# Kernel optimization log

Measured on AMD Instinct MI355X. Metric: run time of the kernel, lower is better.

## Reference

```python
import jax, jax.numpy as jnp
import numpy as np

B, S, D = 2, 2048, 2048
NQ, NKV = 16, 4
HD = D // NQ           # 128
GROUP = NQ // NKV      # 4


def setup_inputs() -> dict:
    key = jax.random.key(0)
    k_x, k_q, k_k, k_v, k_o = jax.random.split(key, 5)
    scale = 0.02
    return {
        "x": jax.random.normal(k_x, (B, S, D), dtype=jnp.float32),
        # torch nn.Linear weights have shape (out_features, in_features)
        "Wq": jax.random.normal(k_q, (D, D), dtype=jnp.float32) * scale,
        "Wk": jax.random.normal(k_k, (NKV * HD, D), dtype=jnp.float32) * scale,
        "Wv": jax.random.normal(k_v, (NKV * HD, D), dtype=jnp.float32) * scale,
        "Wo": jax.random.normal(k_o, (D, D), dtype=jnp.float32) * scale,
    }


def reference(x, Wq, Wk, Wv, Wo):
    b, s, _ = x.shape
    # projections (Linear: x @ W.T), then split heads -> (b, h, s, hd)
    Q = (x @ Wq.T).reshape(b, s, NQ, HD).transpose(0, 2, 1, 3)
    K = (x @ Wk.T).reshape(b, s, NKV, HD).transpose(0, 2, 1, 3)
    V = (x @ Wv.T).reshape(b, s, NKV, HD).transpose(0, 2, 1, 3)
    # GQA: broadcast each KV head across its query-head group (repeat_interleave on head dim)
    K = jnp.repeat(K, GROUP, axis=1)  # (b, NQ, s, hd)
    V = jnp.repeat(V, GROUP, axis=1)
    scores = jnp.einsum("bhqd,bhkd->bhqk", Q, K) / jnp.sqrt(jnp.float32(HD))
    causal = jnp.triu(jnp.ones((s, s), dtype=bool), k=1)  # True above diagonal -> masked
    scores = jnp.where(causal, -jnp.inf, scores)
    weights = jax.nn.softmax(scores, axis=-1)  # dropout p=0.0 -> identity
    ctx = jnp.einsum("bhqk,bhkd->bhqd", weights, V)
    ctx = ctx.transpose(0, 2, 1, 3).reshape(b, s, D)
    return ctx @ Wo.T
```

## Files before the change

kernel.cpp:

```cpp
#include <hip/hip_runtime.h>
#include <stdint.h>

#define S_LEN 2048
#define DMODEL 2048
#define NQH 16
#define NKVH 4
#define HDK 128

typedef __bf16 bf16x8 __attribute__((ext_vector_type(8)));
typedef float f32x4 __attribute__((ext_vector_type(4)));
typedef float f32x16 __attribute__((ext_vector_type(16)));

__device__ __forceinline__ void async16(const void* g, void* l) {
  __builtin_amdgcn_global_load_lds((const __attribute__((address_space(1))) void*)g,
                                   (__attribute__((address_space(3))) void*)l,
                                   16, 0, 0);
}

__device__ __forceinline__ f32x4 mfma16(bf16x8 a, bf16x8 b, f32x4 c) {
  return __builtin_amdgcn_mfma_f32_16x16x32_bf16(a, b, c, 0, 0, 0);
}
__device__ __forceinline__ f32x16 mfma32(bf16x8 a, bf16x8 b, f32x16 c) {
  return __builtin_amdgcn_mfma_f32_32x32x16_bf16(a, b, c, 0, 0, 0);
}
__device__ __forceinline__ uint32_t pkbf16(float lo, float hi) {
  uint32_t r;
  asm("v_cvt_pk_bf16_f32 %0, %1, %2" : "=v"(r) : "v"(lo), "v"(hi));
  return r;
}

__global__ __launch_bounds__(256) void cvt_all(
    const float* __restrict__ i0, const float* __restrict__ i1,
    const float* __restrict__ i2, const float* __restrict__ i3,
    const float* __restrict__ i4, __bf16* __restrict__ o0,
    __bf16* __restrict__ o1, __bf16* __restrict__ o2, __bf16* __restrict__ o3,
    __bf16* __restrict__ o4) {
  int v = blockIdx.x * 256 + threadIdx.x;
  const float* in;
  __bf16* out;
  int base;
  if (v < 1048576)      { in = i0; out = o0; base = 0; }
  else if (v < 1572864) { in = i1; out = o1; base = 1048576; }
  else if (v < 1703936) { in = i2; out = o2; base = 1572864; }
  else if (v < 1835008) { in = i3; out = o3; base = 1703936; }
  else                  { in = i4; out = o4; base = 1835008; }
  int i = (v - base) * 8;
  const float4* p = (const float4*)(in + i);
  float4 a = p[0], b = p[1];
  bf16x8 o;
  o[0] = (__bf16)a.x; o[1] = (__bf16)a.y; o[2] = (__bf16)a.z; o[3] = (__bf16)a.w;
  o[4] = (__bf16)b.x; o[5] = (__bf16)b.y; o[6] = (__bf16)b.z; o[7] = (__bf16)b.w;
  *(bf16x8*)(out + i) = o;
}

template <bool F32OUT, bool VSEG2>
__global__ __launch_bounds__(256) void gemm_bt(const __bf16* __restrict__ A,
                                               const __bf16* __restrict__ B0,
                                               const __bf16* __restrict__ B1,
                                               const __bf16* __restrict__ B2,
                                               void* __restrict__ C0,
                                               void* __restrict__ C1,
                                               void* __restrict__ C2,
                                               int Ntot, int Ns1, int Ns2, int K) {
  int nbn = Ntot >> 7;
  int nwg = gridDim.x;
  int bid = blockIdx.x;
  int bx = (bid & 7) * (nwg >> 3) + (bid >> 3);
  int m0 = (bx / nbn) << 7;
  int n0g = (bx % nbn) << 7;
  const __bf16* B;
  void* C;
  int n0, Nc;
  bool seg2 = false;
  if (n0g < Ns1)      { B = B0; C = C0; n0 = n0g;       Nc = Ns1; }
  else if (n0g < Ns2) { B = B1; C = C1; n0 = n0g - Ns1; Nc = Ns2 - Ns1; }
  else                { B = B2; C = C2; n0 = n0g - Ns2; Nc = Ntot - Ns2; seg2 = true; }

  __shared__ __align__(16) uint8_t As[16384];
  __shared__ __align__(16) uint8_t Bs[16384];

  int t = threadIdx.x, lane = t & 63, w = t >> 6;
  int wr = w >> 1, wc = w & 1;
  f32x4 acc[4][4] = {};

  for (int k0 = 0; k0 < K; k0 += 64) {
#pragma unroll
    for (int i = 0; i < 4; ++i) {
      int c = (i << 8) + t;
      int row = c >> 3;
      int colb = ((c & 7) << 4) ^ ((row & 7) << 4);
      async16((const uint8_t*)(A + (size_t)(m0 + row) * K + k0) + colb, As + c * 16);
      async16((const uint8_t*)(B + (size_t)(n0 + row) * K + k0) + colb, Bs + c * 16);
    }
    __syncthreads();
#pragma unroll
    for (int ks = 0; ks < 2; ++ks) {
      bf16x8 af[4], bfr[4];
#pragma unroll
      for (int m = 0; m < 4; ++m) {
        int row = wr * 64 + m * 16 + (lane & 15);
        int colb = ((ks << 6) + ((lane >> 4) << 4)) ^ ((row & 7) << 4);
        af[m] = *(const bf16x8*)(As + row * 128 + colb);
      }
#pragma unroll
      for (int n = 0; n < 4; ++n) {
        int row = wc * 64 + n * 16 + (lane & 15);
        int colb = ((ks << 6) + ((lane >> 4) << 4)) ^ ((row & 7) << 4);
        bfr[n] = *(const bf16x8*)(Bs + row * 128 + colb);
      }
      __builtin_amdgcn_s_setprio(1);
#pragma unroll
      for (int m = 0; m < 4; ++m)
#pragma unroll
        for (int n = 0; n < 4; ++n)
          acc[m][n] = mfma16(af[m], bfr[n], acc[m][n]);
      __builtin_amdgcn_s_setprio(0);
    }
    __syncthreads();
  }
#pragma unroll
  for (int m = 0; m < 4; ++m)
#pragma unroll
    for (int n = 0; n < 4; ++n)
#pragma unroll
      for (int j = 0; j < 4; ++j) {
        int mg = m0 + wr * 64 + m * 16 + ((lane >> 4) << 2) + j;
        int ng = n0 + wc * 64 + n * 16 + (lane & 15);
        float v = acc[m][n][j];
        if (VSEG2 && seg2) {
          int bb = mg >> 11, s = mg & 2047;
          size_t vidx = ((size_t)((bb << 2) + (ng >> 7)) * 32 + (s >> 6)) * 8192 +
                        (size_t)((s >> 2) & 15) * 512 + (size_t)(ng & 127) * 4 +
                        (s & 3);
          ((__bf16*)C)[vidx] = (__bf16)v;
        } else if (F32OUT) {
          ((float*)C)[(size_t)mg * Nc + ng] = v;
        } else {
          ((__bf16*)C)[(size_t)mg * Nc + ng] = (__bf16)v;
        }
      }
}

__global__ __launch_bounds__(256, 2) void attn(const __bf16* __restrict__ Q,
                                               const __bf16* __restrict__ Kx,
                                               const __bf16* __restrict__ Vt,
                                               __bf16* __restrict__ Ctx) {
  int bid0 = blockIdx.x;
  int bid = ((bid0 & 7) << 6) | (bid0 >> 3);
  int qt = 15 - (bid & 15);
  int h = (bid >> 4) & 15;
  int b = bid >> 8;
  int kvh = h >> 2;
  int q0 = qt << 7;
  int t = threadIdx.x, lane = t & 63, w = t >> 6;
  int qr = lane & 31;
  int hi = lane >> 5;
  int qwb = q0 + (w << 5);

  __shared__ __align__(16) uint8_t Ks[2][16384];
  __shared__ __align__(16) uint8_t Vs[2][16384];

  const __bf16* kbase = Kx + (size_t)b * S_LEN * 512 + kvh * HDK;
  const __bf16* vbase = Vt + (size_t)(b * NKVH + kvh) * 32 * 8192;

  auto stage = [&](int kt, int bufi) {
#pragma unroll
    for (int i = 0; i < 4; ++i) {
      int c = (i << 8) + t;
      int krow = c >> 4;
      int kcolb = ((c & 15) << 4) ^ ((krow & 7) << 4);
      async16((const uint8_t*)(kbase + (size_t)((kt << 6) + krow) * 512) + kcolb,
              Ks[bufi] + c * 16);
      async16((const uint8_t*)(vbase + (size_t)kt * 8192) + c * 16,
              Vs[bufi] + c * 16);
    }
  };

  int NT = (qt << 1) + 2;
  stage(0, 0);

  bf16x8 qf[8];
  {
    const __bf16* qrow = Q + (size_t)(b * S_LEN + qwb + qr) * DMODEL + h * HDK + hi * 8;
#pragma unroll
    for (int dk = 0; dk < 8; ++dk) qf[dk] = *(const bf16x8*)(qrow + dk * 16);
  }
  __syncthreads();

  const float NEG = -3.0e38f;
  const float SC = 0.08838834764831845f;
  float m_run = NEG, l_run = 0.f;
  f32x16 acc[4] = {};

  for (int kt = 0; kt < NT; ++kt) {
    int cur = kt & 1;
    if (kt + 1 < NT) stage(kt + 1, cur ^ 1);
    int k0 = kt << 6;
    if (k0 <= qwb + 31) {
      const uint8_t* ks = Ks[cur];
      const uint8_t* vs = Vs[cur];

      f32x16 st0 = {}, st1 = {};
      __builtin_amdgcn_s_setprio(1);
#pragma unroll
      for (int dk = 0; dk < 8; ++dk) {
        int cb = (dk << 5) + (hi << 4);
        int swz = (qr & 7) << 4;
        bf16x8 kf0 = *(const bf16x8*)(ks + qr * 256 + (cb ^ swz));
        st0 = mfma32(kf0, qf[dk], st0);
        bf16x8 kf1 = *(const bf16x8*)(ks + (32 + qr) * 256 + (cb ^ swz));
        st1 = mfma32(kf1, qf[dk], st1);
      }
      __builtin_amdgcn_s_setprio(0);

      if (k0 + 63 > qwb) {
#pragma unroll
        for (int r = 0; r < 16; ++r) {
          int kl = (r & 3) + ((r >> 2) << 3) + (hi << 2);
          st0[r] = (k0 + kl > qwb + qr) ? NEG : st0[r];
          st1[r] = (k0 + 32 + kl > qwb + qr) ? NEG : st1[r];
        }
      }

      float tm[16];
#pragma unroll
      for (int r = 0; r < 16; ++r) tm[r] = fmaxf(st0[r], st1[r]);
#pragma unroll
      for (int s = 8; s > 0; s >>= 1)
#pragma unroll
        for (int r = 0; r < s; ++r) tm[r] = fmaxf(tm[r], tm[r + s]);
      float mx = fmaxf(tm[0], __shfl_xor(tm[0], 32, 64));

      if (__any(mx > m_run + 90.52f)) {
        float mn = fmaxf(m_run, mx);
        float al = __expf((m_run - mn) * SC);
        l_run *= al;
        m_run = mn;
#pragma unroll
        for (int i = 0; i < 16; ++i) {
          float alr = __shfl(al, (i & 3) + ((i >> 2) << 3) + (hi << 2), 64);
          acc[0][i] *= alr; acc[1][i] *= alr; acc[2][i] *= alr; acc[3][i] *= alr;
        }
      }

      float mSC = m_run * SC;
      float p0[16], p1[16];
#pragma unroll
      for (int r = 0; r < 16; ++r) p0[r] = __expf(fmaf(st0[r], SC, -mSC));
#pragma unroll
      for (int r = 0; r < 16; ++r) p1[r] = __expf(fmaf(st1[r], SC, -mSC));
      float ts[16];
#pragma unroll
      for (int r = 0; r < 16; ++r) ts[r] = p0[r] + p1[r];
#pragma unroll
      for (int s = 8; s > 0; s >>= 1)
#pragma unroll
        for (int r = 0; r < s; ++r) ts[r] += ts[r + s];
      l_run += ts[0];

      bf16x8 pa[4];
      {
        union { bf16x8 v; uint32_t u[4]; } t0, t1, t2, t3;
#pragma unroll
        for (int i = 0; i < 4; ++i) {
          t0.u[i] = pkbf16(p0[2 * i], p0[2 * i + 1]);
          t1.u[i] = pkbf16(p0[8 + 2 * i], p0[9 + 2 * i]);
          t2.u[i] = pkbf16(p1[2 * i], p1[2 * i + 1]);
          t3.u[i] = pkbf16(p1[8 + 2 * i], p1[9 + 2 * i]);
        }
        pa[0] = t0.v; pa[1] = t1.v; pa[2] = t2.v; pa[3] = t3.v;
      }

      __builtin_amdgcn_s_setprio(1);
#pragma unroll
      for (int dt = 0; dt < 4; ++dt) {
        int row = (dt << 5) + qr;
#pragma unroll
        for (int kc = 0; kc < 4; ++kc) {
          int g0 = (kc << 2) + hi;
          union { bf16x8 v; uint64_t q[2]; } vfu;
          vfu.q[0] = *(const uint64_t*)(vs + (g0 << 10) + (row << 3));
          vfu.q[1] = *(const uint64_t*)(vs + ((g0 + 2) << 10) + (row << 3));
          acc[dt] = mfma32(pa[kc], vfu.v, acc[dt]);
        }
      }
      __builtin_amdgcn_s_setprio(0);
    }
    __syncthreads();
  }

  l_run += __shfl_xor(l_run, 32, 64);
#pragma unroll
  for (int i = 0; i < 16; ++i) {
    int rm = (i & 3) + ((i >> 2) << 3) + (hi << 2);
    float lr = __shfl(l_run, rm, 64);
    float inv = 1.0f / lr;
    size_t rowoff = (size_t)(b * S_LEN + qwb + rm) * DMODEL + h * HDK + qr;
#pragma unroll
    for (int dt = 0; dt < 4; ++dt)
      Ctx[rowoff + (dt << 5)] = (__bf16)(acc[dt][i] * inv);
  }
}

extern "C" void kernel_launch(void* const* d_in, const int* in_sizes, int n_in,
                              void* d_out, int out_size, void* d_ws, size_t ws_size,
                              hipStream_t stream) {
  const float* x  = (const float*)d_in[0];
  const float* Wq = (const float*)d_in[1];
  const float* Wk = (const float*)d_in[2];
  const float* Wv = (const float*)d_in[3];
  const float* Wo = (const float*)d_in[4];
  float* out = (float*)d_out;

  const size_t MB = 1024 * 1024;
  uint8_t* ws = (uint8_t*)d_ws;
  __bf16* xb  = (__bf16*)(ws + 0 * MB);
  __bf16* Wqb = (__bf16*)(ws + 16 * MB);
  __bf16* Wkb = (__bf16*)(ws + 24 * MB);
  __bf16* Wvb = (__bf16*)(ws + 26 * MB);
  __bf16* Wob = (__bf16*)(ws + 28 * MB);
  __bf16* Qb  = (__bf16*)(ws + 36 * MB);
  __bf16* Kb  = (__bf16*)(ws + 52 * MB);
  __bf16* Vtb = (__bf16*)(ws + 60 * MB);
  __bf16* Ctx = (__bf16*)(ws + 64 * MB);

  cvt_all<<<9216, 256, 0, stream>>>(x, Wq, Wk, Wv, Wo, xb, Wqb, Wkb, Wvb, Wob);

  gemm_bt<false, true><<<(4096 / 128) * (3072 / 128), 256, 0, stream>>>(
      xb, Wqb, Wkb, Wvb, (void*)Qb, (void*)Kb, (void*)Vtb, 3072, 2048, 2560, 2048);

  attn<<<512, 256, 0, stream>>>(Qb, Kb, Vtb, Ctx);

  gemm_bt<true, false><<<(4096 / 128) * (2048 / 128), 256, 0, stream>>>(
      Ctx, Wob, Wob, Wob, (void*)out, (void*)out, (void*)out, 2048, 2048, 2048, 2048);
}
```

Measured before the change: 191.7 us.

## Software-pipeline QK of next tile with softmax and PV of current tile

Restructures the causal attention loop so that the QK^T MFMAs for tile kt+1 are issued alongside the softmax and PV work for tile kt. To support this, K and V staging are split: K is prefetched two tiles ahead and V one tile ahead. The loop is unrolled by two so the score register sets alternate. The aim is to hide exp/reduction latency behind matrix-core work, at the cost of two extra 16-float accumulator sets per lane, which raises register pressure and may lower occupancy.

```diff
diff --git a/kernel.cpp b/kernel.cpp
--- a/kernel.cpp
+++ b/kernel.cpp
@@ -163,21 +163,29 @@
   const __bf16* kbase = Kx + (size_t)b * S_LEN * 512 + kvh * HDK;
   const __bf16* vbase = Vt + (size_t)(b * NKVH + kvh) * 32 * 8192;
 
-  auto stage = [&](int kt, int bufi) {
+  auto stageK = [&](int kt, int slot) {
 #pragma unroll
     for (int i = 0; i < 4; ++i) {
       int c = (i << 8) + t;
       int krow = c >> 4;
       int kcolb = ((c & 15) << 4) ^ ((krow & 7) << 4);
       async16((const uint8_t*)(kbase + (size_t)((kt << 6) + krow) * 512) + kcolb,
-              Ks[bufi] + c * 16);
+              Ks[slot] + c * 16);
+    }
+  };
+  auto stageV = [&](int kt, int slot) {
+#pragma unroll
+    for (int i = 0; i < 4; ++i) {
+      int c = (i << 8) + t;
       async16((const uint8_t*)(vbase + (size_t)kt * 8192) + c * 16,
-              Vs[bufi] + c * 16);
+              Vs[slot] + c * 16);
     }
   };
 
   int NT = (qt << 1) + 2;
-  stage(0, 0);
+  stageK(0, 0);
+  stageV(0, 0);
+  stageK(1, 1);
 
   bf16x8 qf[8];
   {
@@ -189,104 +197,117 @@
 
   const float NEG = -3.0e38f;
   const float SC = 0.08838834764831845f;
+  const f32x16 vzero = {};
   float m_run = NEG, l_run = 0.f;
   f32x16 acc[4] = {};
 
-  for (int kt = 0; kt < NT; ++kt) {
-    int cur = kt & 1;
-    if (kt + 1 < NT) stage(kt + 1, cur ^ 1);
+  auto qk = [&](int kt, f32x16& n0, f32x16& n1) {
+    const uint8_t* ks = Ks[kt & 1];
+    n0 = vzero; n1 = vzero;
+    int swz = (qr & 7) << 4;
+    __builtin_amdgcn_s_setprio(1);
+#pragma unroll
+    for (int dk = 0; dk < 8; ++dk) {
+      int cb = (dk << 5) + (hi << 4);
+      bf16x8 kf0 = *(const bf16x8*)(ks + qr * 256 + (cb ^ swz));
+      n0 = mfma32(kf0, qf[dk], n0);
+      bf16x8 kf1 = *(const bf16x8*)(ks + (32 + qr) * 256 + (cb ^ swz));
+      n1 = mfma32(kf1, qf[dk], n1);
+    }
+    __builtin_amdgcn_s_setprio(0);
     int k0 = kt << 6;
-    if (k0 <= qwb + 31) {
-      const uint8_t* ks = Ks[cur];
-      const uint8_t* vs = Vs[cur];
-
-      f32x16 st0 = {}, st1 = {};
-      __builtin_amdgcn_s_setprio(1);
-#pragma unroll
-      for (int dk = 0; dk < 8; ++dk) {
-        int cb = (dk << 5) + (hi << 4);
-        int swz = (qr & 7) << 4;
-        bf16x8 kf0 = *(const bf16x8*)(ks + qr * 256 + (cb ^ swz));
-        st0 = mfma32(kf0, qf[dk], st0);
-        bf16x8 kf1 = *(const bf16x8*)(ks + (32 + qr) * 256 + (cb ^ swz));
-        st1 = mfma32(kf1, qf[dk], st1);
-      }
-      __builtin_amdgcn_s_setprio(0);
-
-      if (k0 + 63 > qwb) {
-#pragma unroll
-        for (int r = 0; r < 16; ++r) {
-          int kl = (r & 3) + ((r >> 2) << 3) + (hi << 2);
-          st0[r] = (k0 + kl > qwb + qr) ? NEG : st0[r];
-          st1[r] = (k0 + 32 + kl > qwb + qr) ? NEG : st1[r];
-        }
-      }
-
-      float tm[16];
-#pragma unroll
-      for (int r = 0; r < 16; ++r) tm[r] = fmaxf(st0[r], st1[r]);
-#pragma unroll
-      for (int s = 8; s > 0; s >>= 1)
-#pragma unroll
-        for (int r = 0; r < s; ++r) tm[r] = fmaxf(tm[r], tm[r + s]);
-      float mx = fmaxf(tm[0], __shfl_xor(tm[0], 32, 64));
-
-      if (__any(mx > m_run + 90.52f)) {
-        float mn = fmaxf(m_run, mx);
-        float al = __expf((m_run - mn) * SC);
-        l_run *= al;
-        m_run = mn;
-#pragma unroll
-        for (int i = 0; i < 16; ++i) {
-          float alr = __shfl(al, (i & 3) + ((i >> 2) << 3) + (hi << 2), 64);
-          acc[0][i] *= alr; acc[1][i] *= alr; acc[2][i] *= alr; acc[3][i] *= alr;
-        }
-      }
-
-      float mSC = m_run * SC;
-      float p0[16], p1[16];
-#pragma unroll
-      for (int r = 0; r < 16; ++r) p0[r] = __expf(fmaf(st0[r], SC, -mSC));
-#pragma unroll
-      for (int r = 0; r < 16; ++r) p1[r] = __expf(fmaf(st1[r], SC, -mSC));
-      float ts[16];
-#pragma unroll
-      for (int r = 0; r < 16; ++r) ts[r] = p0[r] + p1[r];
-#pragma unroll
-      for (int s = 8; s > 0; s >>= 1)
-#pragma unroll
-        for (int r = 0; r < s; ++r) ts[r] += ts[r + s];
-      l_run += ts[0];
-
-      bf16x8 pa[4];
-      {
-        union { bf16x8 v; uint32_t u[4]; } t0, t1, t2, t3;
-#pragma unroll
-        for (int i = 0; i < 4; ++i) {
-          t0.u[i] = pkbf16(p0[2 * i], p0[2 * i + 1]);
-          t1.u[i] = pkbf16(p0[8 + 2 * i], p0[9 + 2 * i]);
-          t2.u[i] = pkbf16(p1[2 * i], p1[2 * i + 1]);
-          t3.u[i] = pkbf16(p1[8 + 2 * i], p1[9 + 2 * i]);
-        }
-        pa[0] = t0.v; pa[1] = t1.v; pa[2] = t2.v; pa[3] = t3.v;
-      }
-
-      __builtin_amdgcn_s_setprio(1);
-#pragma unroll
-      for (int dt = 0; dt < 4; ++dt) {
-        int row = (dt << 5) + qr;
-#pragma unroll
-        for (int kc = 0; kc < 4; ++kc) {
-          int g0 = (kc << 2) + hi;
-          union { bf16x8 v; uint64_t q[2]; } vfu;
-          vfu.q[0] = *(const uint64_t*)(vs + (g0 << 10) + (row << 3));
-          vfu.q[1] = *(const uint64_t*)(vs + ((g0 + 2) << 10) + (row << 3));
-          acc[dt] = mfma32(pa[kc], vfu.v, acc[dt]);
-        }
-      }
-      __builtin_amdgcn_s_setprio(0);
-    }
+    if (k0 + 63 > qwb) {
+#pragma unroll
+      for (int r = 0; r < 16; ++r) {
+        int kl = (r & 3) + ((r >> 2) << 3) + (hi << 2);
+        n0[r] = (k0 + kl > qwb + qr) ? NEG : n0[r];
+        n1[r] = (k0 + 32 + kl > qwb + qr) ? NEG : n1[r];
+      }
+    }
+  };
+
+  auto smpv = [&](int kt, f32x16& c0, f32x16& c1) {
+    float tm[16];
+#pragma unroll
+    for (int r = 0; r < 16; ++r) tm[r] = fmaxf(c0[r], c1[r]);
+#pragma unroll
+    for (int s = 8; s > 0; s >>= 1)
+#pragma unroll
+      for (int r = 0; r < s; ++r) tm[r] = fmaxf(tm[r], tm[r + s]);
+    float mx = fmaxf(tm[0], __shfl_xor(tm[0], 32, 64));
+
+    if (__any(mx > m_run + 90.52f)) {
+      float mn = fmaxf(m_run, mx);
+      float al = __expf((m_run - mn) * SC);
+      l_run *= al;
+      m_run = mn;
+#pragma unroll
+      for (int i = 0; i < 16; ++i) {
+        float alr = __shfl(al, (i & 3) + ((i >> 2) << 3) + (hi << 2), 64);
+        acc[0][i] *= alr; acc[1][i] *= alr; acc[2][i] *= alr; acc[3][i] *= alr;
+      }
+    }
+
+    float mSC = m_run * SC;
+    float p0[16], p1[16];
+#pragma unroll
+    for (int r = 0; r < 16; ++r) p0[r] = __expf(fmaf(c0[r], SC, -mSC));
+#pragma unroll
+    for (int r = 0; r < 16; ++r) p1[r] = __expf(fmaf(c1[r], SC, -mSC));
+    float ts[16];
+#pragma unroll
+    for (int r = 0; r < 16; ++r) ts[r] = p0[r] + p1[r];
+#pragma unroll
+    for (int s = 8; s > 0; s >>= 1)
+#pragma unroll
+      for (int r = 0; r < s; ++r) ts[r] += ts[r + s];
+    l_run += ts[0];
+
+    bf16x8 pa[4];
+    {
+      union { bf16x8 v; uint32_t u[4]; } t0, t1, t2, t3;
+#pragma unroll
+      for (int i = 0; i < 4; ++i) {
+        t0.u[i] = pkbf16(p0[2 * i], p0[2 * i + 1]);
+        t1.u[i] = pkbf16(p0[8 + 2 * i], p0[9 + 2 * i]);
+        t2.u[i] = pkbf16(p1[2 * i], p1[2 * i + 1]);
+        t3.u[i] = pkbf16(p1[8 + 2 * i], p1[9 + 2 * i]);
+      }
+      pa[0] = t0.v; pa[1] = t1.v; pa[2] = t2.v; pa[3] = t3.v;
+    }
+
+    const uint8_t* vs = Vs[kt & 1];
+    __builtin_amdgcn_s_setprio(1);
+#pragma unroll
+    for (int dt = 0; dt < 4; ++dt) {
+      int row = (dt << 5) + qr;
+#pragma unroll
+      for (int kc = 0; kc < 4; ++kc) {
+        int g0 = (kc << 2) + hi;
+        union { bf16x8 v; uint64_t q[2]; } vfu;
+        vfu.q[0] = *(const uint64_t*)(vs + (g0 << 10) + (row << 3));
+        vfu.q[1] = *(const uint64_t*)(vs + ((g0 + 2) << 10) + (row << 3));
+        acc[dt] = mfma32(pa[kc], vfu.v, acc[dt]);
+      }
+    }
+    __builtin_amdgcn_s_setprio(0);
+  };
+
+  auto body = [&](int kt, f32x16& c0, f32x16& c1, f32x16& n0, f32x16& n1) {
+    if (kt + 2 < NT) stageK(kt + 2, kt & 1);
+    if (kt + 1 < NT) stageV(kt + 1, (kt + 1) & 1);
+    if (kt + 1 < NT && ((kt + 1) << 6) <= qwb + 31) qk(kt + 1, n0, n1);
+    if ((kt << 6) <= qwb + 31) smpv(kt, c0, c1);
     __syncthreads();
+  };
+
+  f32x16 sA0, sA1, sB0, sB1;
+  qk(0, sA0, sA1);
+  __syncthreads();
+
+  for (int kt = 0; kt < NT; kt += 2) {
+    body(kt, sA0, sA1, sB0, sB1);
+    body(kt + 1, sB0, sB1, sA0, sA1);
   }
 
   l_run += __shfl_xor(l_run, 32, 64);
```

Result: slower. 205.8 us (+7.4%).
